# Kernel tuning notes

Hardware: AMD Instinct MI355X
Metric: run time of the kernel (lower is better)

## Reference

```python
import jax, jax.numpy as jnp
import numpy as np

N_USERS = 100000
N_MOVIES = 20000
N = N_USERS + N_MOVIES
D = 64
N_LAYERS = 3
E = 1000000


def setup_inputs() -> dict:
    key = jax.random.key(0)
    ks = jax.random.split(key, 2 + 4 * N_LAYERS)
    edge_index = jax.random.randint(ks[0], (2, E), 0, N, dtype=jnp.int64)
    emb = jax.random.normal(ks[1], (N, D), dtype=jnp.float32) * 0.1
    scale = 1.0 / np.sqrt(D)
    W1 = jnp.stack([jax.random.uniform(ks[2 + 4 * i], (D, D), jnp.float32, -scale, scale) for i in range(N_LAYERS)])
    b1 = jnp.stack([jax.random.uniform(ks[3 + 4 * i], (D,), jnp.float32, -scale, scale) for i in range(N_LAYERS)])
    W2 = jnp.stack([jax.random.uniform(ks[4 + 4 * i], (D, D), jnp.float32, -scale, scale) for i in range(N_LAYERS)])
    b2 = jnp.stack([jax.random.uniform(ks[5 + 4 * i], (D,), jnp.float32, -scale, scale) for i in range(N_LAYERS)])
    return {"edge_index": edge_index, "emb": emb, "W1": W1, "b1": b1, "W2": W2, "b2": b2}


def _ngcf_conv(x, row, col, norm, W1, b1, W2, b2):
    # gather endpoints: [E, D]
    xr = x[row]
    xc = x[col]
    # msg = norm * (W1(x[col]) + W2(x[row] * x[col]))  (torch Linear: x @ W.T + b)
    msg = norm[:, None] * (xc @ W1.T + b1 + (xr * xc) @ W2.T + b2)
    # scatter_add into row index
    agg = jax.ops.segment_sum(msg, row, num_segments=N)
    # dropout in eval mode = identity; LeakyReLU(0.2)
    return jnp.where(agg >= 0, agg, 0.2 * agg)


def reference(edge_index, emb, W1, b1, W2, b2):
    row, col = edge_index[0], edge_index[1]
    # symmetric degree normalization based on col occurrences (torch_geometric degree(col, N))
    deg = jax.ops.segment_sum(jnp.ones((E,), dtype=emb.dtype), col, num_segments=N)
    dinv = jnp.where(deg > 0, jax.lax.rsqrt(jnp.maximum(deg, 1.0)), 0.0)
    norm = dinv[row] * dinv[col]  # [E]
    x = emb
    all_embs = [x]
    for i in range(N_LAYERS):
        x = _ngcf_conv(x, row, col, norm, W1[i], b1[i], W2[i], b2[i])
        all_embs.append(x)
    return jnp.concatenate(all_embs, axis=1)  # [N, (L+1)*D]
```

## Files before the change

kernel.cpp:

```cpp
#include <hip/hip_runtime.h>

#define NN 120000
#define DD 64
#define EE 1000000
#define NL 3
#define OUTD 256
#define PAD 68
#define NB 469


__global__ void k_degcnt(const int* __restrict__ row, const int* __restrict__ col,
                         int* __restrict__ deg_i, int* __restrict__ cnt) {
    int i = blockIdx.x * blockDim.x + threadIdx.x;
    int stride = gridDim.x * blockDim.x;
    for (int e = i; e < EE; e += stride) {
        atomicAdd(&deg_i[col[e]], 1);
        atomicAdd(&cnt[row[e]], 1);
    }
}

__global__ void k_dinv(const int* __restrict__ deg_i, float* __restrict__ dinv) {
    int n = blockIdx.x * blockDim.x + threadIdx.x;
    if (n < NN) {
        int d = deg_i[n];
        dinv[n] = (d > 0) ? rsqrtf((float)d) : 0.0f;
    }
}

__global__ void k_scanA(const int* __restrict__ cnt, int* __restrict__ row_ptr,
                        int* __restrict__ bsum) {
    __shared__ int sc[256];
    int t = threadIdx.x;
    int i = blockIdx.x * 256 + t;
    int v = (i < NN) ? cnt[i] : 0;
    sc[t] = v;
    __syncthreads();
    for (int off = 1; off < 256; off <<= 1) {
        int u = (t >= off) ? sc[t - off] : 0;
        __syncthreads();
        sc[t] += u;
        __syncthreads();
    }
    if (i < NN) row_ptr[i] = sc[t] - v;
    if (t == 255) bsum[blockIdx.x] = sc[255];
}

__global__ void k_scanB(int* __restrict__ bsum, int* __restrict__ row_ptr) {
    __shared__ int sc[512];
    int t = threadIdx.x;
    int v = (t < NB) ? bsum[t] : 0;
    sc[t] = v;
    __syncthreads();
    for (int off = 1; off < 512; off <<= 1) {
        int u = (t >= off) ? sc[t - off] : 0;
        __syncthreads();
        sc[t] += u;
        __syncthreads();
    }
    if (t < NB) bsum[t] = sc[t] - v;
    if (t == 0) row_ptr[NN] = EE;
}

__global__ void k_scanC(int* __restrict__ row_ptr, const int* __restrict__ bsum) {
    int i = blockIdx.x * blockDim.x + threadIdx.x;
    if (i < NN) row_ptr[i] += bsum[i >> 8];
}

__global__ void k_fill(const int* __restrict__ row, const int* __restrict__ col,
                       const float* __restrict__ dinv, const int* __restrict__ row_ptr,
                       int* __restrict__ fill, float2* __restrict__ csr) {
    int i = blockIdx.x * blockDim.x + threadIdx.x;
    int stride = gridDim.x * blockDim.x;
    for (int e = i; e < EE; e += stride) {
        int r = row[e], c = col[e];
        int pos = row_ptr[r] + atomicAdd(&fill[r], 1);
        csr[pos] = make_float2(__int_as_float(c), dinv[r] * dinv[c]);
    }
}

__global__ void k_copy_emb(const float* __restrict__ emb, float* __restrict__ out) {
    int i = blockIdx.x * blockDim.x + threadIdx.x;
    int stride = gridDim.x * blockDim.x;
    const float4* e4 = (const float4*)emb;
    float4* o4 = (float4*)out;
    const int total = NN * (DD / 4);
    for (int t = i; t < total; t += stride) {
        int n = t / (DD / 4);
        int d4 = t % (DD / 4);
        o4[n * (OUTD / 4) + d4] = e4[t];
    }
}


__global__ void __launch_bounds__(256, 4) k_layer(
    const int* __restrict__ row_ptr, const float2* __restrict__ csr,
    const float* __restrict__ W1, const float* __restrict__ b1,
    const float* __restrict__ W2, const float* __restrict__ b2,
    float* __restrict__ out, int layer)
{
    __shared__ float s1t[64][PAD];
    __shared__ float pt[64][PAD];
    __shared__ float cs[64];

    const int lane = threadIdx.x & 63;
    const int wib  = threadIdx.x >> 6;
    const int n0   = blockIdx.x * 64;
    const float* __restrict__ x = out + layer * DD;
    float* __restrict__ y = out + (layer + 1) * DD;
    const float* __restrict__ W1l = W1 + layer * DD * DD;
    const float* __restrict__ W2l = W2 + layer * DD * DD;

    for (int i = 0; i < 16; ++i) {
        const int nl = wib * 16 + i;
        const int n  = n0 + nl;
        const int beg = row_ptr[n], end = row_ptr[n + 1];
        float acc = 0.f, cacc = 0.f;
        int e = beg;
        for (; e + 4 <= end; e += 4) {
            float2 q0 = csr[e], q1 = csr[e + 1], q2 = csr[e + 2], q3 = csr[e + 3];
            float v0 = x[__float_as_int(q0.x) * OUTD + lane];
            float v1 = x[__float_as_int(q1.x) * OUTD + lane];
            float v2 = x[__float_as_int(q2.x) * OUTD + lane];
            float v3 = x[__float_as_int(q3.x) * OUTD + lane];
            acc += q0.y * v0 + q1.y * v1 + q2.y * v2 + q3.y * v3;
            cacc += q0.y + q1.y + q2.y + q3.y;
        }
        for (; e < end; ++e) {
            float2 q = csr[e];
            acc += q.y * x[__float_as_int(q.x) * OUTD + lane];
            cacc += q.y;
        }
        s1t[nl][lane] = acc;
        pt[nl][lane]  = acc * x[n * OUTD + lane];
        if (lane == 0) cs[nl] = cacc;
    }
    __syncthreads();

    const int tf = threadIdx.x & 15;
    const int tn = threadIdx.x >> 4;
    float acc[4][4];
    #pragma unroll
    for (int i = 0; i < 4; ++i)
        #pragma unroll
        for (int j = 0; j < 4; ++j) acc[i][j] = 0.f;

    for (int k4 = 0; k4 < 16; ++k4) {
        float4 a[4], p[4], wa[4], wb[4];
        #pragma unroll
        for (int i = 0; i < 4; ++i) {
            a[i] = *(const float4*)&s1t[4 * tn + i][4 * k4];
            p[i] = *(const float4*)&pt [4 * tn + i][4 * k4];
        }
        #pragma unroll
        for (int j = 0; j < 4; ++j) {
            wa[j] = *(const float4*)&W1l[(4 * tf + j) * DD + 4 * k4];
            wb[j] = *(const float4*)&W2l[(4 * tf + j) * DD + 4 * k4];
        }
        #pragma unroll
        for (int i = 0; i < 4; ++i)
            #pragma unroll
            for (int j = 0; j < 4; ++j) {
                acc[i][j] += a[i].x * wa[j].x + a[i].y * wa[j].y
                           + a[i].z * wa[j].z + a[i].w * wa[j].w
                           + p[i].x * wb[j].x + p[i].y * wb[j].y
                           + p[i].z * wb[j].z + p[i].w * wb[j].w;
            }
    }

    float bbj[4];
    #pragma unroll
    for (int j = 0; j < 4; ++j) {
        int f = 4 * tf + j;
        bbj[j] = b1[layer * DD + f] + b2[layer * DD + f];
    }
    #pragma unroll
    for (int i = 0; i < 4; ++i) {
        int nl = 4 * tn + i;
        float c = cs[nl];
        float4 r;
        float t0 = acc[i][0] + c * bbj[0]; r.x = t0 >= 0.f ? t0 : 0.2f * t0;
        float t1 = acc[i][1] + c * bbj[1]; r.y = t1 >= 0.f ? t1 : 0.2f * t1;
        float t2 = acc[i][2] + c * bbj[2]; r.z = t2 >= 0.f ? t2 : 0.2f * t2;
        float t3 = acc[i][3] + c * bbj[3]; r.w = t3 >= 0.f ? t3 : 0.2f * t3;
        *(float4*)&y[(n0 + nl) * OUTD + 4 * tf] = r;
    }
}


extern "C" void kernel_launch(void* const* d_in, const int* in_sizes, int n_in,
                              void* d_out, int out_size, void* d_ws, size_t ws_size,
                              hipStream_t stream) {
    const int*   ei  = (const int*)d_in[0];
    const float* emb = (const float*)d_in[1];
    const float* W1  = (const float*)d_in[2];
    const float* b1  = (const float*)d_in[3];
    const float* W2  = (const float*)d_in[4];
    const float* b2  = (const float*)d_in[5];
    float* out = (float*)d_out;

    const int* row = ei;
    const int* col = ei + EE;

    float2* csr   = (float2*)d_ws;
    int* ibase    = (int*)(csr + EE);
    int* deg_i    = ibase;
    int* cnt      = deg_i + NN;
    int* fill     = cnt + NN;
    int* row_ptr  = fill + NN;
    int* bsum     = row_ptr + NN + 1;
    float* dinv   = (float*)(bsum + 512);

    hipMemsetAsync(ibase, 0, (size_t)3 * NN * sizeof(int), stream);

    k_degcnt<<<1024, 256, 0, stream>>>(row, col, deg_i, cnt);
    k_dinv<<<NB, 256, 0, stream>>>(deg_i, dinv);
    k_scanA<<<NB, 256, 0, stream>>>(cnt, row_ptr, bsum);
    k_scanB<<<1, 512, 0, stream>>>(bsum, row_ptr);
    k_scanC<<<NB, 256, 0, stream>>>(row_ptr, bsum);
    k_fill<<<1024, 256, 0, stream>>>(row, col, dinv, row_ptr, fill, csr);
    k_copy_emb<<<2048, 256, 0, stream>>>(emb, out);

    for (int layer = 0; layer < NL; ++layer) {
        k_layer<<<NN / 64, 256, 0, stream>>>(row_ptr, csr, W1, b1, W2, b2, out, layer);
    }
}
```

Before: 884.4 us.

## Balance per-block edge gather across waves with LDS atomics and factor out dinv

The layer kernel now splits each 64-node block's contiguous CSR edge range evenly across its four waves instead of giving each wave 16 fixed nodes. Partial sums are accumulated with shared-memory atomics, using the local node id packed into the low bits of the column index. The row-side dinv factor is applied after aggregation, and the per-node norm sum is precomputed once in the fill kernel via global atomics. This removes one LDS tile and raises launch bounds occupancy, but adds LDS atomic contention and a float atomic per edge during CSR construction.

```diff
diff --git a/kernel.cpp b/kernel.cpp
--- a/kernel.cpp
+++ b/kernel.cpp
@@ -68,13 +68,16 @@
 
 __global__ void k_fill(const int* __restrict__ row, const int* __restrict__ col,
                        const float* __restrict__ dinv, const int* __restrict__ row_ptr,
-                       int* __restrict__ fill, float2* __restrict__ csr) {
+                       int* __restrict__ fill, float2* __restrict__ csr,
+                       float* __restrict__ cbuf) {
     int i = blockIdx.x * blockDim.x + threadIdx.x;
     int stride = gridDim.x * blockDim.x;
     for (int e = i; e < EE; e += stride) {
         int r = row[e], c = col[e];
+        float dr = dinv[r], dc = dinv[c];
         int pos = row_ptr[r] + atomicAdd(&fill[r], 1);
-        csr[pos] = make_float2(__int_as_float(c), dinv[r] * dinv[c]);
+        csr[pos] = make_float2(__int_as_float((c << 6) | (r & 63)), dc);
+        atomicAdd(&cbuf[r], dr * dc);
     }
 }
 
@@ -85,86 +88,96 @@
     float4* o4 = (float4*)out;
     const int total = NN * (DD / 4);
     for (int t = i; t < total; t += stride) {
-        int n = t / (DD / 4);
-        int d4 = t % (DD / 4);
+        int n = t >> 4;
+        int d4 = t & 15;
         o4[n * (OUTD / 4) + d4] = e4[t];
     }
 }
 
 
-__global__ void __launch_bounds__(256, 4) k_layer(
+__global__ void __launch_bounds__(256, 6) k_layer(
     const int* __restrict__ row_ptr, const float2* __restrict__ csr,
+    const float* __restrict__ dinv, const float* __restrict__ cbuf,
     const float* __restrict__ W1, const float* __restrict__ b1,
     const float* __restrict__ W2, const float* __restrict__ b2,
     float* __restrict__ out, int layer)
 {
     __shared__ float s1t[64][PAD];
-    __shared__ float pt[64][PAD];
-    __shared__ float cs[64];
 
     const int lane = threadIdx.x & 63;
     const int wib  = threadIdx.x >> 6;
     const int n0   = blockIdx.x * 64;
     const float* __restrict__ x = out + layer * DD;
-    float* __restrict__ y = out + (layer + 1) * DD;
+
+    #pragma unroll
+    for (int i = 0; i < 16; ++i) s1t[wib * 16 + i][lane] = 0.f;
+    __syncthreads();
+
+    const int beg = row_ptr[n0];
+    const int end = row_ptr[n0 + 64];
+    const int per = (end - beg + 3) >> 2;
+    int e0 = beg + wib * per;
+    int e1 = min(end, e0 + per);
+
+    int e = e0;
+    for (; e + 8 <= e1; e += 8) {
+        float2 q[8];
+        #pragma unroll
+        for (int u = 0; u < 8; ++u) q[u] = csr[e + u];
+        float v[8];
+        #pragma unroll
+        for (int u = 0; u < 8; ++u)
+            v[u] = q[u].y * x[(__float_as_int(q[u].x) >> 6) * OUTD + lane];
+        #pragma unroll
+        for (int u = 0; u < 8; ++u)
+            atomicAdd(&s1t[__float_as_int(q[u].x) & 63][lane], v[u]);
+    }
+    for (; e < e1; ++e) {
+        float2 q = csr[e];
+        float v = q.y * x[(__float_as_int(q.x) >> 6) * OUTD + lane];
+        atomicAdd(&s1t[__float_as_int(q.x) & 63][lane], v);
+    }
+    __syncthreads();
+
+    const int tf = threadIdx.x & 15;
+    const int tn = threadIdx.x >> 4;
     const float* __restrict__ W1l = W1 + layer * DD * DD;
     const float* __restrict__ W2l = W2 + layer * DD * DD;
 
-    for (int i = 0; i < 16; ++i) {
-        const int nl = wib * 16 + i;
-        const int n  = n0 + nl;
-        const int beg = row_ptr[n], end = row_ptr[n + 1];
-        float acc = 0.f, cacc = 0.f;
-        int e = beg;
-        for (; e + 4 <= end; e += 4) {
-            float2 q0 = csr[e], q1 = csr[e + 1], q2 = csr[e + 2], q3 = csr[e + 3];
-            float v0 = x[__float_as_int(q0.x) * OUTD + lane];
-            float v1 = x[__float_as_int(q1.x) * OUTD + lane];
-            float v2 = x[__float_as_int(q2.x) * OUTD + lane];
-            float v3 = x[__float_as_int(q3.x) * OUTD + lane];
-            acc += q0.y * v0 + q1.y * v1 + q2.y * v2 + q3.y * v3;
-            cacc += q0.y + q1.y + q2.y + q3.y;
+    float dv[4];
+    #pragma unroll
+    for (int i = 0; i < 4; ++i) dv[i] = dinv[n0 + 4 * tn + i];
+
+    float acc[4][4];
+    #pragma unroll
+    for (int i = 0; i < 4; ++i)
+        #pragma unroll
+        for (int j = 0; j < 4; ++j) acc[i][j] = 0.f;
+
+    for (int k4 = 0; k4 < 16; ++k4) {
+        float4 a[4], p[4];
+        #pragma unroll
+        for (int i = 0; i < 4; ++i) {
+            int nl = 4 * tn + i;
+            float4 s  = *(const float4*)&s1t[nl][4 * k4];
+            float4 xv = *(const float4*)&x[(size_t)(n0 + nl) * OUTD + 4 * k4];
+            a[i].x = s.x * dv[i]; a[i].y = s.y * dv[i];
+            a[i].z = s.z * dv[i]; a[i].w = s.w * dv[i];
+            p[i].x = a[i].x * xv.x; p[i].y = a[i].y * xv.y;
+            p[i].z = a[i].z * xv.z; p[i].w = a[i].w * xv.w;
         }
-        for (; e < end; ++e) {
-            float2 q = csr[e];
-            acc += q.y * x[__float_as_int(q.x) * OUTD + lane];
-            cacc += q.y;
+        #pragma unroll
+        for (int j = 0; j < 4; ++j) {
+            float4 wa = *(const float4*)&W1l[(4 * tf + j) * DD + 4 * k4];
+            float4 wb = *(const float4*)&W2l[(4 * tf + j) * DD + 4 * k4];
+            #pragma unroll
+            for (int i = 0; i < 4; ++i) {
+                acc[i][j] += a[i].x * wa.x + a[i].y * wa.y
+                           + a[i].z * wa.z + a[i].w * wa.w
+                           + p[i].x * wb.x + p[i].y * wb.y
+                           + p[i].z * wb.z + p[i].w * wb.w;
+            }
         }
-        s1t[nl][lane] = acc;
-        pt[nl][lane]  = acc * x[n * OUTD + lane];
-        if (lane == 0) cs[nl] = cacc;
-    }
-    __syncthreads();
-
-    const int tf = threadIdx.x & 15;
-    const int tn = threadIdx.x >> 4;
-    float acc[4][4];
-    #pragma unroll
-    for (int i = 0; i < 4; ++i)
-        #pragma unroll
-        for (int j = 0; j < 4; ++j) acc[i][j] = 0.f;
-
-    for (int k4 = 0; k4 < 16; ++k4) {
-        float4 a[4], p[4], wa[4], wb[4];
-        #pragma unroll
-        for (int i = 0; i < 4; ++i) {
-            a[i] = *(const float4*)&s1t[4 * tn + i][4 * k4];
-            p[i] = *(const float4*)&pt [4 * tn + i][4 * k4];
-        }
-        #pragma unroll
-        for (int j = 0; j < 4; ++j) {
-            wa[j] = *(const float4*)&W1l[(4 * tf + j) * DD + 4 * k4];
-            wb[j] = *(const float4*)&W2l[(4 * tf + j) * DD + 4 * k4];
-        }
-        #pragma unroll
-        for (int i = 0; i < 4; ++i)
-            #pragma unroll
-            for (int j = 0; j < 4; ++j) {
-                acc[i][j] += a[i].x * wa[j].x + a[i].y * wa[j].y
-                           + a[i].z * wa[j].z + a[i].w * wa[j].w
-                           + p[i].x * wb[j].x + p[i].y * wb[j].y
-                           + p[i].z * wb[j].z + p[i].w * wb[j].w;
-            }
     }
 
     float bbj[4];
@@ -175,14 +188,14 @@
     }
     #pragma unroll
     for (int i = 0; i < 4; ++i) {
-        int nl = 4 * tn + i;
-        float c = cs[nl];
+        int n = n0 + 4 * tn + i;
+        float c = cbuf[n];
         float4 r;
         float t0 = acc[i][0] + c * bbj[0]; r.x = t0 >= 0.f ? t0 : 0.2f * t0;
         float t1 = acc[i][1] + c * bbj[1]; r.y = t1 >= 0.f ? t1 : 0.2f * t1;
         float t2 = acc[i][2] + c * bbj[2]; r.z = t2 >= 0.f ? t2 : 0.2f * t2;
         float t3 = acc[i][3] + c * bbj[3]; r.w = t3 >= 0.f ? t3 : 0.2f * t3;
-        *(float4*)&y[(n0 + nl) * OUTD + 4 * tf] = r;
+        *(float4*)&out[(size_t)n * OUTD + (layer + 1) * DD + 4 * tf] = r;
     }
 }
 
@@ -201,26 +214,28 @@
     const int* row = ei;
     const int* col = ei + EE;
 
-    float2* csr   = (float2*)d_ws;
-    int* ibase    = (int*)(csr + EE);
-    int* deg_i    = ibase;
-    int* cnt      = deg_i + NN;
-    int* fill     = cnt + NN;
-    int* row_ptr  = fill + NN;
-    int* bsum     = row_ptr + NN + 1;
-    float* dinv   = (float*)(bsum + 512);
-
-    hipMemsetAsync(ibase, 0, (size_t)3 * NN * sizeof(int), stream);
+    float2* csr  = (float2*)d_ws;
+    int* ibase   = (int*)(csr + EE);
+    int* deg_i   = ibase;
+    int* cnt     = deg_i + NN;
+    int* fill    = cnt + NN;
+    float* cbuf  = (float*)(fill + NN);
+    int* row_ptr = (int*)(cbuf + NN);
+    int* bsum    = row_ptr + NN + 1;
+    float* dinv  = (float*)(bsum + 512);
+
+    hipMemsetAsync(ibase, 0, (size_t)4 * NN * sizeof(int), stream);
 
     k_degcnt<<<1024, 256, 0, stream>>>(row, col, deg_i, cnt);
     k_dinv<<<NB, 256, 0, stream>>>(deg_i, dinv);
     k_scanA<<<NB, 256, 0, stream>>>(cnt, row_ptr, bsum);
     k_scanB<<<1, 512, 0, stream>>>(bsum, row_ptr);
     k_scanC<<<NB, 256, 0, stream>>>(row_ptr, bsum);
-    k_fill<<<1024, 256, 0, stream>>>(row, col, dinv, row_ptr, fill, csr);
+    k_fill<<<1024, 256, 0, stream>>>(row, col, dinv, row_ptr, fill, csr, cbuf);
     k_copy_emb<<<2048, 256, 0, stream>>>(emb, out);
 
     for (int layer = 0; layer < NL; ++layer) {
-        k_layer<<<NN / 64, 256, 0, stream>>>(row_ptr, csr, W1, b1, W2, b2, out, layer);
-    }
-}
+        k_layer<<<NN / 64, 256, 0, stream>>>(row_ptr, csr, dinv, cbuf,
+                                             W1, b1, W2, b2, out, layer);
+    }
+}
```

New measurement: 1.724 ms. 94.9% more time.
